# Kernel optimization log

Measured on AMD Instinct MI355X. Metric: run time of the kernel, lower is better.

Reference implementation:

```python
import jax, jax.numpy as jnp
import numpy as np
from jax import lax

B, C, N, T, K = 16, 64, 512, 64, 3
EPS = 1e-5


def _bn(x, g, b):
    # training-mode BatchNorm2d over (B, H=N, W=T) per channel
    m = jnp.mean(x, axis=(0, 2, 3), keepdims=True)
    v = jnp.var(x, axis=(0, 2, 3), keepdims=True)
    return (x - m) * lax.rsqrt(v + EPS) * g[None, :, None, None] + b[None, :, None, None]


def _conv(x, w, b, pad):
    y = lax.conv_general_dilated(x, w, (1, 1), ((0, 0), pad),
                                 dimension_numbers=('NCHW', 'OIHW', 'NCHW'))
    return y + b[None, :, None, None]


def setup_inputs() -> dict:
    key = jax.random.key(0)
    ks = jax.random.split(key, 8)
    xav = lambda k, sh, fi, fo: jax.random.normal(k, sh, jnp.float32) * np.sqrt(2.0 / (fi + fo))
    return {
        'x': jax.random.normal(ks[0], (B, C, N, T), jnp.float32),
        'adj_mx': jax.random.normal(ks[1], (K, N, N), jnp.float32) / np.sqrt(N),
        'cheb_w': xav(ks[2], (K, C, C), C, C),
        'cheb_b': jnp.zeros((C,), jnp.float32),
        'w1': xav(ks[3], (C, C, 1, 3), 3 * C, 3 * C),
        'b1': jnp.zeros((C,), jnp.float32),
        'g1': jnp.ones((C,), jnp.float32),
        'be1': jnp.zeros((C,), jnp.float32),
        'w2': xav(ks[4], (C, C, 1, 3), 3 * C, 3 * C),
        'b2': jnp.zeros((C,), jnp.float32),
        'g2': jnp.ones((C,), jnp.float32),
        'be2': jnp.zeros((C,), jnp.float32),
        'gate_w': xav(ks[5], (C, 2 * C, 1, 1), 2 * C, C),
        'gate_b': jnp.zeros((C,), jnp.float32),
        'res_w': xav(ks[6], (C, C, 1, 1), C, C),
        'res_b': jnp.zeros((C,), jnp.float32),
        'g3': jnp.ones((C,), jnp.float32),
        'be3': jnp.zeros((C,), jnp.float32),
    }


def _forward(x, adj_mx, cheb_w, cheb_b, w1, b1, g1, be1, w2, b2, g2, be2,
             gate_w, gate_b, res_w, res_b, g3, be3):
    # ChebFilterBlock: out[b,o,n,t] = sum_{k,i,m} x[b,i,m,t] adj[k,m,n] W[k,i,o] + bias
    spatial = jnp.einsum('bimt,kmn,kio->bont', x, adj_mx, cheb_w) \
              + cheb_b[None, :, None, None]
    # temporal branch: two (1,3) convs with BN+ReLU
    t = jax.nn.relu(_bn(_conv(x, w1, b1, (1, 1)), g1, be1))
    t = jax.nn.relu(_bn(_conv(t, w2, b2, (1, 1)), g2, be2))
    # gated fusion
    comb = jnp.concatenate([spatial, t], axis=1)
    gate = jax.nn.sigmoid(_conv(comb, gate_w, gate_b, (0, 0)))
    res = _conv(x, res_w, res_b, (0, 0))
    out = gate * spatial + (1.0 - gate) * t + res
    return _bn(out, g3, be3)


def reference(x, adj_mx, cheb_w, cheb_b, w1, b1, g1, be1, w2, b2, g2, be2,
              gate_w, gate_b, res_w, res_b, g3, be3):
    return _forward(x, adj_mx, cheb_w, cheb_b, w1, b1, g1, be1, w2, b2, g2, be2,
                    gate_w, gate_b, res_w, res_b, g3, be3)
```

## Files before the change

kernel.cpp:

```cpp
#include <hip/hip_runtime.h>
#include <hip/hip_bf16.h>
#include <cstdint>

#define BB 16
#define CC 64
#define NN 512
#define TT 64
#define KCH 3
#define PP (BB*NN*TT)
#define EPSB 1e-5f

typedef __bf16 bf16;
typedef __bf16 bf16x8 __attribute__((ext_vector_type(8)));
typedef __bf16 bf16x4 __attribute__((ext_vector_type(4)));
typedef float  f32x4  __attribute__((ext_vector_type(4)));

#define MFMA16(A,Bv,Cv) __builtin_amdgcn_mfma_f32_16x16x32_bf16((A),(Bv),(Cv),0,0,0)

__device__ __forceinline__ void gload_lds16(const bf16* g, bf16* l){
  __builtin_amdgcn_global_load_lds(
      (const __attribute__((address_space(1))) void*)g,
      (__attribute__((address_space(3))) void*)l, 16, 0, 0);
}

__global__ __launch_bounds__(256) void k_prep(const float* __restrict__ adj,
    const float* __restrict__ w1, const float* __restrict__ w2,
    const float* __restrict__ cw, const float* __restrict__ gw,
    const float* __restrict__ rw, bf16* __restrict__ adjb,
    bf16* __restrict__ w1p, bf16* __restrict__ w2p, bf16* __restrict__ cp,
    bf16* __restrict__ gp, bf16* __restrict__ rp){
  int blk = blockIdx.x, tid = threadIdx.x;
  if (blk < 3072){
    int idx = blk*256 + tid;
    int m = idx & 511, n = (idx >> 9) & 511, k = idx >> 18;
    adjb[idx] = (bf16)adj[((size_t)(k*512 + m))*512 + n];
    return;
  }
  int e0 = (blk - 3072)*256 + tid;
  if (e0 < 12288){
    int e = e0;
    int j = e&7, lane = (e>>3)&63, cf = (e>>9)&3, ks = e>>11;
    int k = ks*32 + (lane>>4)*8 + j, col = cf*16 + (lane&15);
    int kk = k >> 6, i = k & 63;
    w1p[e] = (bf16)w1[(col*64 + i)*3 + kk];
    w2p[e] = (bf16)w2[(col*64 + i)*3 + kk];
    cp[e]  = (bf16)cw[((size_t)kk*64 + i)*64 + col];
  } else if (e0 < 20480){
    int e = e0 - 12288;
    int j = e&7, lane = (e>>3)&63, cf = (e>>9)&3, ks = e>>11;
    int k = ks*32 + (lane>>4)*8 + j, col = cf*16 + (lane&15);
    gp[e] = (bf16)gw[col*128 + k];
  } else {
    int e = e0 - 20480;
    int j = e&7, lane = (e>>3)&63, cf = (e>>9)&3, ks = e>>11;
    int k = ks*32 + (lane>>4)*8 + j, col = cf*16 + (lane&15);
    rp[e] = (bf16)rw[col*64 + k];
  }
}

__global__ __launch_bounds__(256) void k_xprep(const float* __restrict__ x,
    bf16* __restrict__ xlb, bf16* __restrict__ xmt){
  __shared__ bf16 T[32768];
  int bid = blockIdx.x;
  int b = bid >> 6, i0 = ((bid >> 3) & 7)*8, n0 = (bid & 7)*64;
  int tid = threadIdx.x;
  #pragma unroll 4
  for (int it = 0; it < 32; ++it){
    int flat = it*256 + tid;
    int t4 = flat & 15, n = (flat >> 4) & 63, i = flat >> 10;
    float4 v = *reinterpret_cast<const float4*>(
        x + ((size_t)((b*64 + i0 + i)*512) + (n0 + n))*64 + t4*4);
    int s = t4 ^ ((n + 2*i) & 15);
    bf16x4 pk; pk[0]=(bf16)v.x; pk[1]=(bf16)v.y; pk[2]=(bf16)v.z; pk[3]=(bf16)v.w;
    *reinterpret_cast<bf16x4*>(&T[(i*64 + n)*64 + s*4]) = pk;
  }
  __syncthreads();
  #pragma unroll 4
  for (int it = 0; it < 16; ++it){
    int flat = it*256 + tid;
    int mc = flat & 7, i = (flat >> 3) & 7, t = flat >> 6;
    bf16x8 o;
    #pragma unroll
    for (int e = 0; e < 8; ++e){
      int m = mc*8 + e;
      int s = (t >> 2) ^ ((m + 2*i) & 15);
      o[e] = T[(i*64 + m)*64 + s*4 + (t & 3)];
    }
    *reinterpret_cast<bf16x8*>(
        &xmt[((size_t)((b*64 + t)*64) + i0 + i)*512 + n0 + mc*8]) = o;
  }
  #pragma unroll 4
  for (int it = 0; it < 16; ++it){
    int flat = it*256 + tid;
    int t = flat & 63, n = flat >> 6;
    bf16x8 o;
    #pragma unroll
    for (int e = 0; e < 8; ++e){
      int s = (t >> 2) ^ ((n + 2*e) & 15);
      o[e] = T[(e*64 + n)*64 + s*4 + (t & 3)];
    }
    *reinterpret_cast<bf16x8*>(
        &xlb[(((size_t)b*512 + n0 + n)*64 + t)*64 + i0]) = o;
  }
}

__global__ __launch_bounds__(256,4) void k_conv(const bf16* __restrict__ in,
    const bf16* __restrict__ wp, bf16* __restrict__ outp, float* __restrict__ part,
    const float* __restrict__ sc, const float* __restrict__ sh){
  int tid = threadIdx.x, w = tid >> 6, l = tid & 63, l15 = l & 15, lg = l >> 4;
  int blk = blockIdx.x;
  size_t rowbase = (size_t)blk * 64;
  const bf16* xr = in + rowbase * 64;
  int t = w*16 + l15;
  f32x4 acc[4] = {};
  #pragma unroll
  for (int ks = 0; ks < 6; ++ks){
    int dt = ks >> 1, kh = ks & 1;
    int ts = t + dt - 1;
    bf16x8 a = {};
    if (ts >= 0 && ts < 64){
      a = *reinterpret_cast<const bf16x8*>(xr + ts*64 + kh*32 + lg*8);
      if (sc){
        int i0 = kh*32 + lg*8;
        #pragma unroll
        for (int e = 0; e < 8; ++e){
          float f = (float)a[e]*sc[i0+e] + sh[i0+e];
          a[e] = (bf16)fmaxf(f, 0.f);
        }
      }
    }
    #pragma unroll
    for (int cf = 0; cf < 4; ++cf){
      bf16x8 bfr = *reinterpret_cast<const bf16x8*>(wp + ((ks*4 + cf)*64 + l)*8);
      acc[cf] = MFMA16(a, bfr, acc[cf]);
    }
  }
  __shared__ float ssum[4][4][16], ssq[4][4][16];
  #pragma unroll
  for (int cf = 0; cf < 4; ++cf){
    int o = cf*16 + l15;
    float s = 0.f, q = 0.f;
    #pragma unroll
    for (int r = 0; r < 4; ++r){
      float vv = acc[cf][r];
      int to = w*16 + lg*4 + r;
      outp[(rowbase + to)*64 + o] = (bf16)vv;
      s += vv; q += vv*vv;
    }
    s += __shfl_xor(s, 16); s += __shfl_xor(s, 32);
    q += __shfl_xor(q, 16); q += __shfl_xor(q, 32);
    if (lg == 0){ ssum[w][cf][l15] = s; ssq[w][cf][l15] = q; }
  }
  __syncthreads();
  if (tid < 64){
    int cf = tid >> 4, c = tid & 15;
    float s = ssum[0][cf][c]+ssum[1][cf][c]+ssum[2][cf][c]+ssum[3][cf][c];
    float q = ssq[0][cf][c]+ssq[1][cf][c]+ssq[2][cf][c]+ssq[3][cf][c];
    part[(size_t)blk*128 + tid*2]     = s;
    part[(size_t)blk*128 + tid*2 + 1] = q;
  }
}

__global__ __launch_bounds__(256) void k_stats(const float* __restrict__ part, int nb,
    const float* __restrict__ g, const float* __restrict__ be,
    float* __restrict__ sc, float* __restrict__ sh){
  int c = blockIdx.x, tid = threadIdx.x;
  float s = 0.f, q = 0.f;
  for (int i = tid; i < nb; i += 256){
    s += part[(size_t)i*128 + c*2];
    q += part[(size_t)i*128 + c*2 + 1];
  }
  __shared__ float rs[256], rq[256];
  rs[tid] = s; rq[tid] = q; __syncthreads();
  for (int st = 128; st > 0; st >>= 1){
    if (tid < st){ rs[tid] += rs[tid+st]; rq[tid] += rq[tid+st]; }
    __syncthreads();
  }
  if (tid == 0){
    float cnt = (float)PP;
    float mean = rs[0]/cnt, var = rq[0]/cnt - mean*mean;
    float r = rsqrtf(var + EPSB);
    sc[c] = g[c]*r;
    sh[c] = be[c] - mean*g[c]*r;
  }
}

__global__ __launch_bounds__(512,2) void k_gemm1(const bf16* __restrict__ xmt,
    const bf16* __restrict__ adjb, const bf16* __restrict__ cp,
    const float* __restrict__ cb, bf16* __restrict__ spm){
  __shared__ __align__(16) bf16 LDS[32768];

  int tid = threadIdx.x, w = tid >> 6, l = tid & 63, l15 = l & 15, lg = l >> 4;
  int wm = w >> 2, wn2 = w & 3;

  int orig = blockIdx.x;
  int wg = (orig & 7) * 256 + (orig >> 3);
  int jt = wg >> 2, nt = wg & 3;
  int J0 = jt*128, N0 = nt*128;

  const bf16* aglob = xmt + (size_t)J0*512;
  const bf16* bglob = adjb + (size_t)N0*512;

  int srow = tid >> 3, scn = (tid & 7) ^ ((tid >> 3) & 7);
  size_t soff = (size_t)srow*512 + scn*8;

  int colx[2];
  #pragma unroll
  for (int ph = 0; ph < 2; ++ph) colx[ph] = ((ph*4 + lg) ^ (l15 & 7))*8;
  int aoff[4], boff[2];
  #pragma unroll
  for (int jf = 0; jf < 4; ++jf) aoff[jf] = (wm*64 + jf*16 + l15)*64;
  #pragma unroll
  for (int nf = 0; nf < 2; ++nf) boff[nf] = (wn2*32 + nf*16 + l15)*64;

  f32x4 acc[4][2];
  f32x4 acc2[2][4] = {};

  for (int kk = 0; kk < 3; ++kk){
    const bf16* bko = bglob + (size_t)kk*262144;
    #pragma unroll
    for (int jf = 0; jf < 4; ++jf)
      #pragma unroll
      for (int nf = 0; nf < 2; ++nf)
        acc[jf][nf] = (f32x4){0.f,0.f,0.f,0.f};

    gload_lds16(aglob + soff,          LDS + tid*8);
    gload_lds16(aglob + soff + 32768,  LDS + 4096 + tid*8);
    gload_lds16(bko   + soff,          LDS + 16384 + tid*8);
    gload_lds16(bko   + soff + 32768,  LDS + 16384 + 4096 + tid*8);

    for (int kt = 0; kt < 8; ++kt){
      int buf = kt & 1, nbuf = buf ^ 1;
      bf16* Ab = LDS + buf*8192;
      bf16* Bb = LDS + 16384 + buf*8192;
      int mnext = (kt+1)*64;
      #pragma unroll
      for (int ph = 0; ph < 2; ++ph){
        if (kt < 7){
          if (ph == 0){
            gload_lds16(aglob + soff + mnext,         LDS + nbuf*8192 + tid*8);
            gload_lds16(aglob + soff + 32768 + mnext, LDS + nbuf*8192 + 4096 + tid*8);
          } else {
            gload_lds16(bko + soff + mnext,           LDS + 16384 + nbuf*8192 + tid*8);
            gload_lds16(bko + soff + 32768 + mnext,   LDS + 16384 + nbuf*8192 + 4096 + tid*8);
          }
        }
        if (ph == 0){
          if (kt < 7) asm volatile("s_waitcnt vmcnt(2)" ::: "memory");
          else        asm volatile("s_waitcnt vmcnt(0)" ::: "memory");
        }
        __builtin_amdgcn_sched_barrier(0);
        __builtin_amdgcn_s_barrier();
        __builtin_amdgcn_sched_barrier(0);

        bf16x8 a[4], bfr[2];
        #pragma unroll
        for (int jf = 0; jf < 4; ++jf)
          a[jf] = *reinterpret_cast<const bf16x8*>(&Ab[aoff[jf] + colx[ph]]);
        #pragma unroll
        for (int nf = 0; nf < 2; ++nf)
          bfr[nf] = *reinterpret_cast<const bf16x8*>(&Bb[boff[nf] + colx[ph]]);

        __builtin_amdgcn_s_setprio(1);
        #pragma unroll
        for (int jf = 0; jf < 4; ++jf)
          #pragma unroll
          for (int nf = 0; nf < 2; ++nf)
            acc[jf][nf] = MFMA16(a[jf], bfr[nf], acc[jf][nf]);
        __builtin_amdgcn_s_setprio(0);

        asm volatile("s_waitcnt lgkmcnt(0)" ::: "memory");
        __builtin_amdgcn_sched_barrier(0);
        __builtin_amdgcn_s_barrier();
      }
    }

    char* VTb = (char*)LDS;
    #pragma unroll
    for (int jf = 0; jf < 4; ++jf){
      int jb16 = wm*8 + jf*2 + (lg >> 1);
      int jlow = lg & 1;
      #pragma unroll
      for (int nf = 0; nf < 2; ++nf){
        int n = wn2*32 + nf*16 + l15;
        bf16x4 pk;
        #pragma unroll
        for (int r = 0; r < 4; ++r) pk[r] = (bf16)acc[jf][nf][r];
        *reinterpret_cast<bf16x4*>(
            VTb + n*256 + ((jb16 ^ (n & 15)) << 4) + (jlow << 3)) = pk;
      }
    }
    asm volatile("s_waitcnt lgkmcnt(0)" ::: "memory");
    __builtin_amdgcn_sched_barrier(0);
    __builtin_amdgcn_s_barrier();

    {
      int tloc = w >> 2, nbase = (w & 3)*32;
      #pragma unroll
      for (int ks2 = 0; ks2 < 2; ++ks2){
        bf16x8 bc[4];
        #pragma unroll
        for (int cf = 0; cf < 4; ++cf)
          bc[cf] = *reinterpret_cast<const bf16x8*>(
              cp + (((kk*2 + ks2)*4 + cf)*64 + l)*8);
        #pragma unroll
        for (int rf2 = 0; rf2 < 2; ++rf2){
          int nloc = nbase + rf2*16 + l15;
          int jb16 = tloc*8 + ks2*4 + lg;
          bf16x8 a2 = *reinterpret_cast<const bf16x8*>(
              VTb + nloc*256 + ((jb16 ^ (nloc & 15)) << 4));
          #pragma unroll
          for (int cf = 0; cf < 4; ++cf)
            acc2[rf2][cf] = MFMA16(a2, bc[cf], acc2[rf2][cf]);
        }
      }
    }
    asm volatile("s_waitcnt lgkmcnt(0)" ::: "memory");
    __builtin_amdgcn_sched_barrier(0);
    __builtin_amdgcn_s_barrier();
  }

  __syncthreads();
  bf16* SP = LDS;
  float cbv[4];
  #pragma unroll
  for (int cf = 0; cf < 4; ++cf) cbv[cf] = cb[cf*16 + l15];
  {
    int tloc = w >> 2, nbase = (w & 3)*32;
    #pragma unroll
    for (int rf2 = 0; rf2 < 2; ++rf2){
      int rowb = tloc*128 + nbase + rf2*16 + lg*4;
      #pragma unroll
      for (int cf = 0; cf < 4; ++cf){
        int o = cf*16 + l15;
        #pragma unroll
        for (int r = 0; r < 4; ++r)
          SP[(rowb + r)*64 + o] = (bf16)(acc2[rf2][cf][r] + cbv[cf]);
      }
    }
  }
  __syncthreads();
  int b = jt >> 5, t0 = (jt & 31)*2;
  #pragma unroll
  for (int q = 0; q < 4; ++q){
    int flat = q*512 + tid;
    int row = flat >> 3, oc = (flat & 7)*8;
    int tl = row >> 7, n = N0 + (row & 127);
    bf16x8 vv = *reinterpret_cast<const bf16x8*>(&SP[row*64 + oc]);
    *reinterpret_cast<bf16x8*>(
        &spm[(((size_t)b*512 + n)*64 + (t0 + tl))*64 + oc]) = vv;
  }
}

__global__ __launch_bounds__(256,4) void k_fusion(const bf16* __restrict__ spm,
    const bf16* __restrict__ t2, const bf16* __restrict__ xlb,
    const bf16* __restrict__ gp, const bf16* __restrict__ rp,
    const float* __restrict__ sc2, const float* __restrict__ sh2,
    const float* __restrict__ gateb, bf16* __restrict__ pre,
    float* __restrict__ part){
  int tid = threadIdx.x, w = tid >> 6, l = tid & 63, l15 = l & 15, lg = l >> 4;
  int blk = blockIdx.x;
  int b = blk >> 9, n = blk & 511;
  size_t rowbase = (size_t)blk * 64;
  int t = w*16 + l15;
  f32x4 ag[4] = {}, ar[4] = {};
  #pragma unroll
  for (int ks = 0; ks < 4; ++ks){
    bf16x8 a;
    if (ks < 2){
      a = *reinterpret_cast<const bf16x8*>(spm + (rowbase + t)*64 + ks*32 + lg*8);
    } else {
      int i0 = (ks-2)*32 + lg*8;
      bf16x8 raw = *reinterpret_cast<const bf16x8*>(t2 + (rowbase + t)*64 + i0);
      #pragma unroll
      for (int e = 0; e < 8; ++e){
        float f = (float)raw[e]*sc2[i0+e] + sh2[i0+e];
        a[e] = (bf16)fmaxf(f, 0.f);
      }
    }
    #pragma unroll
    for (int cf = 0; cf < 4; ++cf){
      bf16x8 bfr = *reinterpret_cast<const bf16x8*>(gp + ((ks*4 + cf)*64 + l)*8);
      ag[cf] = MFMA16(a, bfr, ag[cf]);
    }
  }
  #pragma unroll
  for (int ks = 0; ks < 2; ++ks){
    bf16x8 a = *reinterpret_cast<const bf16x8*>(xlb + (rowbase + t)*64 + ks*32 + lg*8);
    #pragma unroll
    for (int cf = 0; cf < 4; ++cf){
      bf16x8 bfr = *reinterpret_cast<const bf16x8*>(rp + ((ks*4 + cf)*64 + l)*8);
      ar[cf] = MFMA16(a, bfr, ar[cf]);
    }
  }
  __shared__ float ssum[4][4][16], ssq[4][4][16];
  int tb = w*16 + lg*4;
  #pragma unroll
  for (int cf = 0; cf < 4; ++cf){
    int o = cf*16 + l15;
    float gb = gateb[o], sco = sc2[o], sho = sh2[o];
    float s = 0.f, q = 0.f;
    bf16x4 ov;
    #pragma unroll
    for (int r = 0; r < 4; ++r){
      size_t row = rowbase + tb + r;
      float z = ag[cf][r] + gb;
      float g = 1.f/(1.f + __expf(-z));
      float spv = (float)spm[row*64 + o];
      float tv  = (float)t2[row*64 + o];
      tv = fmaxf(tv*sco + sho, 0.f);
      float val = g*spv + (1.f - g)*tv + ar[cf][r];
      ov[r] = (bf16)val;
      s += val; q += val*val;
    }
    *reinterpret_cast<bf16x4*>(pre + (((size_t)b*64 + o)*512 + n)*64 + tb) = ov;
    s += __shfl_xor(s, 16); s += __shfl_xor(s, 32);
    q += __shfl_xor(q, 16); q += __shfl_xor(q, 32);
    if (lg == 0){ ssum[w][cf][l15] = s; ssq[w][cf][l15] = q; }
  }
  __syncthreads();
  if (tid < 64){
    int cf = tid >> 4, c = tid & 15;
    float s = ssum[0][cf][c]+ssum[1][cf][c]+ssum[2][cf][c]+ssum[3][cf][c];
    float q = ssq[0][cf][c]+ssq[1][cf][c]+ssq[2][cf][c]+ssq[3][cf][c];
    part[(size_t)blk*128 + tid*2]     = s;
    part[(size_t)blk*128 + tid*2 + 1] = q;
  }
}

__global__ __launch_bounds__(256) void k_bn3(const bf16* __restrict__ pre,
    float* __restrict__ out,
    const float* __restrict__ sc, const float* __restrict__ sh){
  size_t total8 = (size_t)BB*CC*NN*TT/8;
  for (size_t i8 = (size_t)blockIdx.x*256 + threadIdx.x; i8 < total8;
       i8 += (size_t)gridDim.x*256){
    bf16x8 v = reinterpret_cast<const bf16x8*>(pre)[i8];
    int o = (int)(i8 >> 12) & 63;
    float a = sc[o], bsh = sh[o];
    float4 r0, r1;
    r0.x = (float)v[0]*a + bsh; r0.y = (float)v[1]*a + bsh;
    r0.z = (float)v[2]*a + bsh; r0.w = (float)v[3]*a + bsh;
    r1.x = (float)v[4]*a + bsh; r1.y = (float)v[5]*a + bsh;
    r1.z = (float)v[6]*a + bsh; r1.w = (float)v[7]*a + bsh;
    reinterpret_cast<float4*>(out)[i8*2]     = r0;
    reinterpret_cast<float4*>(out)[i8*2 + 1] = r1;
  }
}

extern "C" void kernel_launch(void* const* d_in, const int* in_sizes, int n_in,
                              void* d_out, int out_size, void* d_ws, size_t ws_size,
                              hipStream_t stream){
  (void)in_sizes; (void)n_in; (void)out_size; (void)ws_size;
  const float* x   = (const float*)d_in[0];
  const float* adj = (const float*)d_in[1];
  const float* cw  = (const float*)d_in[2];
  const float* cb  = (const float*)d_in[3];
  const float* w1  = (const float*)d_in[4];
  const float* g1  = (const float*)d_in[6];
  const float* be1 = (const float*)d_in[7];
  const float* w2  = (const float*)d_in[8];
  const float* g2  = (const float*)d_in[10];
  const float* be2 = (const float*)d_in[11];
  const float* gw  = (const float*)d_in[12];
  const float* gb  = (const float*)d_in[13];
  const float* rw  = (const float*)d_in[14];
  const float* g3  = (const float*)d_in[16];
  const float* be3 = (const float*)d_in[17];
  float* out = (float*)d_out;

  char* ws = (char*)d_ws;
  size_t off = 0;
  auto alloc = [&](size_t bytes)->char*{
    char* p = ws + off; off += (bytes + 255) & ~(size_t)255; return p;
  };
  bf16* xlb  = (bf16*)alloc((size_t)PP*64*2);
  bf16* xmt  = (bf16*)alloc((size_t)PP*64*2);
  bf16* t1   = (bf16*)alloc((size_t)PP*64*2);
  bf16* t2   = (bf16*)alloc((size_t)PP*64*2);
  bf16* spm  = t1;
  bf16* pre  = xmt;
  bf16* adjb = (bf16*)alloc((size_t)KCH*512*512*2);
  bf16* w1p  = (bf16*)alloc(6*2048*2);
  bf16* w2p  = (bf16*)alloc(6*2048*2);
  bf16* cp   = (bf16*)alloc(6*2048*2);
  bf16* gp   = (bf16*)alloc(4*2048*2);
  bf16* rp   = (bf16*)alloc(2*2048*2);
  float* part = (float*)alloc((size_t)8192*128*4);
  float* s1sc = (float*)alloc(256); float* s1sh = (float*)alloc(256);
  float* s2sc = (float*)alloc(256); float* s2sh = (float*)alloc(256);
  float* s3sc = (float*)alloc(256); float* s3sh = (float*)alloc(256);

  k_prep <<<dim3(3168), dim3(256), 0, stream>>>(adj, w1, w2, cw, gw, rw,
                                                adjb, w1p, w2p, cp, gp, rp);
  k_xprep<<<dim3(1024), dim3(256), 0, stream>>>(x, xlb, xmt);

  k_conv <<<dim3(8192), dim3(256), 0, stream>>>(xlb, w1p, t1, part, nullptr, nullptr);
  k_stats<<<dim3(64),   dim3(256), 0, stream>>>(part, 8192, g1, be1, s1sc, s1sh);
  k_conv <<<dim3(8192), dim3(256), 0, stream>>>(t1, w2p, t2, part, s1sc, s1sh);
  k_stats<<<dim3(64),   dim3(256), 0, stream>>>(part, 8192, g2, be2, s2sc, s2sh);

  k_gemm1<<<dim3(2048), dim3(512), 0, stream>>>(xmt, adjb, cp, cb, spm);

  k_fusion<<<dim3(8192), dim3(256), 0, stream>>>(spm, t2, xlb, gp, rp,
                                                 s2sc, s2sh, gb, pre, part);
  k_stats<<<dim3(64),   dim3(256), 0, stream>>>(part, 8192, g3, be3, s3sc, s3sh);
  k_bn3  <<<dim3(2048), dim3(256), 0, stream>>>(pre, out, s3sc, s3sh);
}
```

Measured before the change: 549.0 us.

## Split spatial GEMM into halves co-scheduled with each temporal conv launch

The separate conv and Chebyshev GEMM kernels are merged into one heterogeneous kernel. The first 1024 blocks run half of the GEMM tiles and the remaining blocks run the (1,3) conv, with two conv rows per 512-thread block. The kernel is launched twice, once per conv layer, so the compute-bound GEMM can overlap with the memory-bound conv passes and one launch is removed. The spatial output now gets its own buffer instead of aliasing t1, which costs extra workspace. Conv blocks now carry the GEMM's 64 KB static LDS and 512-thread launch bounds, which may reduce conv occupancy.

```diff
diff --git a/kernel.cpp b/kernel.cpp
--- a/kernel.cpp
+++ b/kernel.cpp
@@ -104,63 +104,6 @@
   }
 }
 
-__global__ __launch_bounds__(256,4) void k_conv(const bf16* __restrict__ in,
-    const bf16* __restrict__ wp, bf16* __restrict__ outp, float* __restrict__ part,
-    const float* __restrict__ sc, const float* __restrict__ sh){
-  int tid = threadIdx.x, w = tid >> 6, l = tid & 63, l15 = l & 15, lg = l >> 4;
-  int blk = blockIdx.x;
-  size_t rowbase = (size_t)blk * 64;
-  const bf16* xr = in + rowbase * 64;
-  int t = w*16 + l15;
-  f32x4 acc[4] = {};
-  #pragma unroll
-  for (int ks = 0; ks < 6; ++ks){
-    int dt = ks >> 1, kh = ks & 1;
-    int ts = t + dt - 1;
-    bf16x8 a = {};
-    if (ts >= 0 && ts < 64){
-      a = *reinterpret_cast<const bf16x8*>(xr + ts*64 + kh*32 + lg*8);
-      if (sc){
-        int i0 = kh*32 + lg*8;
-        #pragma unroll
-        for (int e = 0; e < 8; ++e){
-          float f = (float)a[e]*sc[i0+e] + sh[i0+e];
-          a[e] = (bf16)fmaxf(f, 0.f);
-        }
-      }
-    }
-    #pragma unroll
-    for (int cf = 0; cf < 4; ++cf){
-      bf16x8 bfr = *reinterpret_cast<const bf16x8*>(wp + ((ks*4 + cf)*64 + l)*8);
-      acc[cf] = MFMA16(a, bfr, acc[cf]);
-    }
-  }
-  __shared__ float ssum[4][4][16], ssq[4][4][16];
-  #pragma unroll
-  for (int cf = 0; cf < 4; ++cf){
-    int o = cf*16 + l15;
-    float s = 0.f, q = 0.f;
-    #pragma unroll
-    for (int r = 0; r < 4; ++r){
-      float vv = acc[cf][r];
-      int to = w*16 + lg*4 + r;
-      outp[(rowbase + to)*64 + o] = (bf16)vv;
-      s += vv; q += vv*vv;
-    }
-    s += __shfl_xor(s, 16); s += __shfl_xor(s, 32);
-    q += __shfl_xor(q, 16); q += __shfl_xor(q, 32);
-    if (lg == 0){ ssum[w][cf][l15] = s; ssq[w][cf][l15] = q; }
-  }
-  __syncthreads();
-  if (tid < 64){
-    int cf = tid >> 4, c = tid & 15;
-    float s = ssum[0][cf][c]+ssum[1][cf][c]+ssum[2][cf][c]+ssum[3][cf][c];
-    float q = ssq[0][cf][c]+ssq[1][cf][c]+ssq[2][cf][c]+ssq[3][cf][c];
-    part[(size_t)blk*128 + tid*2]     = s;
-    part[(size_t)blk*128 + tid*2 + 1] = q;
-  }
-}
-
 __global__ __launch_bounds__(256) void k_stats(const float* __restrict__ part, int nb,
     const float* __restrict__ g, const float* __restrict__ be,
     float* __restrict__ sc, float* __restrict__ sh){
@@ -185,170 +128,241 @@
   }
 }
 
-__global__ __launch_bounds__(512,2) void k_gemm1(const bf16* __restrict__ xmt,
-    const bf16* __restrict__ adjb, const bf16* __restrict__ cp,
-    const float* __restrict__ cb, bf16* __restrict__ spm){
+__global__ __launch_bounds__(512,2) void k_fat(
+    const bf16* __restrict__ cin, const bf16* __restrict__ wp,
+    bf16* __restrict__ coutp, float* __restrict__ part,
+    const float* __restrict__ sc, const float* __restrict__ sh,
+    const bf16* __restrict__ xmt, const bf16* __restrict__ adjb,
+    const bf16* __restrict__ cp, const float* __restrict__ cb,
+    bf16* __restrict__ spm, int gofs){
   __shared__ __align__(16) bf16 LDS[32768];
 
-  int tid = threadIdx.x, w = tid >> 6, l = tid & 63, l15 = l & 15, lg = l >> 4;
-  int wm = w >> 2, wn2 = w & 3;
-
-  int orig = blockIdx.x;
-  int wg = (orig & 7) * 256 + (orig >> 3);
-  int jt = wg >> 2, nt = wg & 3;
-  int J0 = jt*128, N0 = nt*128;
-
-  const bf16* aglob = xmt + (size_t)J0*512;
-  const bf16* bglob = adjb + (size_t)N0*512;
-
-  int srow = tid >> 3, scn = (tid & 7) ^ ((tid >> 3) & 7);
-  size_t soff = (size_t)srow*512 + scn*8;
-
-  int colx[2];
-  #pragma unroll
-  for (int ph = 0; ph < 2; ++ph) colx[ph] = ((ph*4 + lg) ^ (l15 & 7))*8;
-  int aoff[4], boff[2];
-  #pragma unroll
-  for (int jf = 0; jf < 4; ++jf) aoff[jf] = (wm*64 + jf*16 + l15)*64;
-  #pragma unroll
-  for (int nf = 0; nf < 2; ++nf) boff[nf] = (wn2*32 + nf*16 + l15)*64;
-
-  f32x4 acc[4][2];
-  f32x4 acc2[2][4] = {};
-
-  for (int kk = 0; kk < 3; ++kk){
-    const bf16* bko = bglob + (size_t)kk*262144;
-    #pragma unroll
-    for (int jf = 0; jf < 4; ++jf)
-      #pragma unroll
-      for (int nf = 0; nf < 2; ++nf)
-        acc[jf][nf] = (f32x4){0.f,0.f,0.f,0.f};
-
-    gload_lds16(aglob + soff,          LDS + tid*8);
-    gload_lds16(aglob + soff + 32768,  LDS + 4096 + tid*8);
-    gload_lds16(bko   + soff,          LDS + 16384 + tid*8);
-    gload_lds16(bko   + soff + 32768,  LDS + 16384 + 4096 + tid*8);
-
-    for (int kt = 0; kt < 8; ++kt){
-      int buf = kt & 1, nbuf = buf ^ 1;
-      bf16* Ab = LDS + buf*8192;
-      bf16* Bb = LDS + 16384 + buf*8192;
-      int mnext = (kt+1)*64;
-      #pragma unroll
-      for (int ph = 0; ph < 2; ++ph){
-        if (kt < 7){
+  int blk = blockIdx.x;
+  int tid = threadIdx.x;
+
+  if (blk < 1024){
+    int w = tid >> 6, l = tid & 63, l15 = l & 15, lg = l >> 4;
+    int wm = w >> 2, wn2 = w & 3;
+
+    int gwg = blk + gofs;
+    int wg = (gwg & 7) * 256 + (gwg >> 3);
+    int jt = wg >> 2, nt = wg & 3;
+    int J0 = jt*128, N0 = nt*128;
+
+    const bf16* aglob = xmt + (size_t)J0*512;
+    const bf16* bglob = adjb + (size_t)N0*512;
+
+    int srow = tid >> 3, scn = (tid & 7) ^ ((tid >> 3) & 7);
+    size_t soff = (size_t)srow*512 + scn*8;
+
+    int colx[2];
+    #pragma unroll
+    for (int ph = 0; ph < 2; ++ph) colx[ph] = ((ph*4 + lg) ^ (l15 & 7))*8;
+    int aoff[4], boff[2];
+    #pragma unroll
+    for (int jf = 0; jf < 4; ++jf) aoff[jf] = (wm*64 + jf*16 + l15)*64;
+    #pragma unroll
+    for (int nf = 0; nf < 2; ++nf) boff[nf] = (wn2*32 + nf*16 + l15)*64;
+
+    f32x4 acc[4][2];
+    f32x4 acc2[2][4] = {};
+
+    for (int kk = 0; kk < 3; ++kk){
+      const bf16* bko = bglob + (size_t)kk*262144;
+      #pragma unroll
+      for (int jf = 0; jf < 4; ++jf)
+        #pragma unroll
+        for (int nf = 0; nf < 2; ++nf)
+          acc[jf][nf] = (f32x4){0.f,0.f,0.f,0.f};
+
+      gload_lds16(aglob + soff,          LDS + tid*8);
+      gload_lds16(aglob + soff + 32768,  LDS + 4096 + tid*8);
+      gload_lds16(bko   + soff,          LDS + 16384 + tid*8);
+      gload_lds16(bko   + soff + 32768,  LDS + 16384 + 4096 + tid*8);
+
+      for (int kt = 0; kt < 8; ++kt){
+        int buf = kt & 1, nbuf = buf ^ 1;
+        bf16* Ab = LDS + buf*8192;
+        bf16* Bb = LDS + 16384 + buf*8192;
+        int mnext = (kt+1)*64;
+        #pragma unroll
+        for (int ph = 0; ph < 2; ++ph){
+          if (kt < 7){
+            if (ph == 0){
+              gload_lds16(cin ? aglob + soff + mnext : aglob, LDS + nbuf*8192 + tid*8);
+              gload_lds16(aglob + soff + 32768 + mnext, LDS + nbuf*8192 + 4096 + tid*8);
+            } else {
+              gload_lds16(bko + soff + mnext,           LDS + 16384 + nbuf*8192 + tid*8);
+              gload_lds16(bko + soff + 32768 + mnext,   LDS + 16384 + nbuf*8192 + 4096 + tid*8);
+            }
+          }
           if (ph == 0){
-            gload_lds16(aglob + soff + mnext,         LDS + nbuf*8192 + tid*8);
-            gload_lds16(aglob + soff + 32768 + mnext, LDS + nbuf*8192 + 4096 + tid*8);
-          } else {
-            gload_lds16(bko + soff + mnext,           LDS + 16384 + nbuf*8192 + tid*8);
-            gload_lds16(bko + soff + 32768 + mnext,   LDS + 16384 + nbuf*8192 + 4096 + tid*8);
+            if (kt < 7) asm volatile("s_waitcnt vmcnt(2)" ::: "memory");
+            else        asm volatile("s_waitcnt vmcnt(0)" ::: "memory");
+          }
+          __builtin_amdgcn_sched_barrier(0);
+          __builtin_amdgcn_s_barrier();
+          __builtin_amdgcn_sched_barrier(0);
+
+          bf16x8 a[4], bfr[2];
+          #pragma unroll
+          for (int jf = 0; jf < 4; ++jf)
+            a[jf] = *reinterpret_cast<const bf16x8*>(&Ab[aoff[jf] + colx[ph]]);
+          #pragma unroll
+          for (int nf = 0; nf < 2; ++nf)
+            bfr[nf] = *reinterpret_cast<const bf16x8*>(&Bb[boff[nf] + colx[ph]]);
+
+          __builtin_amdgcn_s_setprio(1);
+          #pragma unroll
+          for (int jf = 0; jf < 4; ++jf)
+            #pragma unroll
+            for (int nf = 0; nf < 2; ++nf)
+              acc[jf][nf] = MFMA16(a[jf], bfr[nf], acc[jf][nf]);
+          __builtin_amdgcn_s_setprio(0);
+
+          asm volatile("s_waitcnt lgkmcnt(0)" ::: "memory");
+          __builtin_amdgcn_sched_barrier(0);
+          __builtin_amdgcn_s_barrier();
+        }
+      }
+
+      char* VTb = (char*)LDS;
+      #pragma unroll
+      for (int jf = 0; jf < 4; ++jf){
+        int jb16 = wm*8 + jf*2 + (lg >> 1);
+        int jlow = lg & 1;
+        #pragma unroll
+        for (int nf = 0; nf < 2; ++nf){
+          int n = wn2*32 + nf*16 + l15;
+          bf16x4 pk;
+          #pragma unroll
+          for (int r = 0; r < 4; ++r) pk[r] = (bf16)acc[jf][nf][r];
+          *reinterpret_cast<bf16x4*>(
+              VTb + n*256 + ((jb16 ^ (n & 15)) << 4) + (jlow << 3)) = pk;
+        }
+      }
+      asm volatile("s_waitcnt lgkmcnt(0)" ::: "memory");
+      __builtin_amdgcn_sched_barrier(0);
+      __builtin_amdgcn_s_barrier();
+
+      {
+        int tloc = w >> 2, nbase = (w & 3)*32;
+        #pragma unroll
+        for (int ks2 = 0; ks2 < 2; ++ks2){
+          bf16x8 bc[4];
+          #pragma unroll
+          for (int cf = 0; cf < 4; ++cf)
+            bc[cf] = *reinterpret_cast<const bf16x8*>(
+                cp + (((kk*2 + ks2)*4 + cf)*64 + l)*8);
+          #pragma unroll
+          for (int rf2 = 0; rf2 < 2; ++rf2){
+            int nloc = nbase + rf2*16 + l15;
+            int jb16 = tloc*8 + ks2*4 + lg;
+            bf16x8 a2 = *reinterpret_cast<const bf16x8*>(
+                VTb + nloc*256 + ((jb16 ^ (nloc & 15)) << 4));
+            #pragma unroll
+            for (int cf = 0; cf < 4; ++cf)
+              acc2[rf2][cf] = MFMA16(a2, bc[cf], acc2[rf2][cf]);
           }
         }
-        if (ph == 0){
-          if (kt < 7) asm volatile("s_waitcnt vmcnt(2)" ::: "memory");
-          else        asm volatile("s_waitcnt vmcnt(0)" ::: "memory");
-        }
-        __builtin_amdgcn_sched_barrier(0);
-        __builtin_amdgcn_s_barrier();
-        __builtin_amdgcn_sched_barrier(0);
-
-        bf16x8 a[4], bfr[2];
-        #pragma unroll
-        for (int jf = 0; jf < 4; ++jf)
-          a[jf] = *reinterpret_cast<const bf16x8*>(&Ab[aoff[jf] + colx[ph]]);
-        #pragma unroll
-        for (int nf = 0; nf < 2; ++nf)
-          bfr[nf] = *reinterpret_cast<const bf16x8*>(&Bb[boff[nf] + colx[ph]]);
-
-        __builtin_amdgcn_s_setprio(1);
-        #pragma unroll
-        for (int jf = 0; jf < 4; ++jf)
-          #pragma unroll
-          for (int nf = 0; nf < 2; ++nf)
-            acc[jf][nf] = MFMA16(a[jf], bfr[nf], acc[jf][nf]);
-        __builtin_amdgcn_s_setprio(0);
-
-        asm volatile("s_waitcnt lgkmcnt(0)" ::: "memory");
-        __builtin_amdgcn_sched_barrier(0);
-        __builtin_amdgcn_s_barrier();
-      }
-    }
-
-    char* VTb = (char*)LDS;
-    #pragma unroll
-    for (int jf = 0; jf < 4; ++jf){
-      int jb16 = wm*8 + jf*2 + (lg >> 1);
-      int jlow = lg & 1;
-      #pragma unroll
-      for (int nf = 0; nf < 2; ++nf){
-        int n = wn2*32 + nf*16 + l15;
-        bf16x4 pk;
-        #pragma unroll
-        for (int r = 0; r < 4; ++r) pk[r] = (bf16)acc[jf][nf][r];
-        *reinterpret_cast<bf16x4*>(
-            VTb + n*256 + ((jb16 ^ (n & 15)) << 4) + (jlow << 3)) = pk;
-      }
-    }
-    asm volatile("s_waitcnt lgkmcnt(0)" ::: "memory");
-    __builtin_amdgcn_sched_barrier(0);
-    __builtin_amdgcn_s_barrier();
-
+      }
+      asm volatile("s_waitcnt lgkmcnt(0)" ::: "memory");
+      __builtin_amdgcn_sched_barrier(0);
+      __builtin_amdgcn_s_barrier();
+    }
+
+    __syncthreads();
+    bf16* SP = LDS;
+    float cbv[4];
+    #pragma unroll
+    for (int cf = 0; cf < 4; ++cf) cbv[cf] = cb[cf*16 + l15];
     {
       int tloc = w >> 2, nbase = (w & 3)*32;
       #pragma unroll
-      for (int ks2 = 0; ks2 < 2; ++ks2){
-        bf16x8 bc[4];
+      for (int rf2 = 0; rf2 < 2; ++rf2){
+        int rowb = tloc*128 + nbase + rf2*16 + lg*4;
         #pragma unroll
-        for (int cf = 0; cf < 4; ++cf)
-          bc[cf] = *reinterpret_cast<const bf16x8*>(
-              cp + (((kk*2 + ks2)*4 + cf)*64 + l)*8);
-        #pragma unroll
-        for (int rf2 = 0; rf2 < 2; ++rf2){
-          int nloc = nbase + rf2*16 + l15;
-          int jb16 = tloc*8 + ks2*4 + lg;
-          bf16x8 a2 = *reinterpret_cast<const bf16x8*>(
-              VTb + nloc*256 + ((jb16 ^ (nloc & 15)) << 4));
-          #pragma unroll
-          for (int cf = 0; cf < 4; ++cf)
-            acc2[rf2][cf] = MFMA16(a2, bc[cf], acc2[rf2][cf]);
+        for (int cf = 0; cf < 4; ++cf){
+          int o = cf*16 + l15;
+          #pragma unroll
+          for (int r = 0; r < 4; ++r)
+            SP[(rowb + r)*64 + o] = (bf16)(acc2[rf2][cf][r] + cbv[cf]);
         }
       }
     }
-    asm volatile("s_waitcnt lgkmcnt(0)" ::: "memory");
-    __builtin_amdgcn_sched_barrier(0);
-    __builtin_amdgcn_s_barrier();
-  }
-
-  __syncthreads();
-  bf16* SP = LDS;
-  float cbv[4];
-  #pragma unroll
-  for (int cf = 0; cf < 4; ++cf) cbv[cf] = cb[cf*16 + l15];
-  {
-    int tloc = w >> 2, nbase = (w & 3)*32;
-    #pragma unroll
-    for (int rf2 = 0; rf2 < 2; ++rf2){
-      int rowb = tloc*128 + nbase + rf2*16 + lg*4;
+    __syncthreads();
+    int b = jt >> 5, t0 = (jt & 31)*2;
+    #pragma unroll
+    for (int q = 0; q < 4; ++q){
+      int flat = q*512 + tid;
+      int row = flat >> 3, oc = (flat & 7)*8;
+      int tl = row >> 7, n = N0 + (row & 127);
+      bf16x8 vv = *reinterpret_cast<const bf16x8*>(&SP[row*64 + oc]);
+      *reinterpret_cast<bf16x8*>(
+          &spm[(((size_t)b*512 + n)*64 + (t0 + tl))*64 + oc]) = vv;
+    }
+  } else {
+    int sub = tid >> 8, t8 = tid & 255;
+    int w = t8 >> 6, l = t8 & 63, l15 = l & 15, lg = l >> 4;
+    size_t bn = (size_t)(blk - 1024)*2 + sub;
+    size_t rowbase = bn * 64;
+    const bf16* xr = cin + rowbase * 64;
+    int t = w*16 + l15;
+    f32x4 acc[4] = {};
+    #pragma unroll
+    for (int ks = 0; ks < 6; ++ks){
+      int dt = ks >> 1, kh = ks & 1;
+      int ts = t + dt - 1;
+      bf16x8 a = {};
+      if (ts >= 0 && ts < 64){
+        a = *reinterpret_cast<const bf16x8*>(xr + ts*64 + kh*32 + lg*8);
+        if (sc){
+          int i0 = kh*32 + lg*8;
+          #pragma unroll
+          for (int e = 0; e < 8; ++e){
+            float f = (float)a[e]*sc[i0+e] + sh[i0+e];
+            a[e] = (bf16)fmaxf(f, 0.f);
+          }
+        }
+      }
       #pragma unroll
       for (int cf = 0; cf < 4; ++cf){
-        int o = cf*16 + l15;
-        #pragma unroll
-        for (int r = 0; r < 4; ++r)
-          SP[(rowb + r)*64 + o] = (bf16)(acc2[rf2][cf][r] + cbv[cf]);
-      }
-    }
-  }
-  __syncthreads();
-  int b = jt >> 5, t0 = (jt & 31)*2;
-  #pragma unroll
-  for (int q = 0; q < 4; ++q){
-    int flat = q*512 + tid;
-    int row = flat >> 3, oc = (flat & 7)*8;
-    int tl = row >> 7, n = N0 + (row & 127);
-    bf16x8 vv = *reinterpret_cast<const bf16x8*>(&SP[row*64 + oc]);
-    *reinterpret_cast<bf16x8*>(
-        &spm[(((size_t)b*512 + n)*64 + (t0 + tl))*64 + oc]) = vv;
+        bf16x8 bfr = *reinterpret_cast<const bf16x8*>(wp + ((ks*4 + cf)*64 + l)*8);
+        acc[cf] = MFMA16(a, bfr, acc[cf]);
+      }
+    }
+    float* ssum = (float*)LDS;
+    float* ssq  = ssum + 512;
+    #pragma unroll
+    for (int cf = 0; cf < 4; ++cf){
+      int o = cf*16 + l15;
+      float s = 0.f, q = 0.f;
+      #pragma unroll
+      for (int r = 0; r < 4; ++r){
+        float vv = acc[cf][r];
+        int to = w*16 + lg*4 + r;
+        coutp[(rowbase + to)*64 + o] = (bf16)vv;
+        s += vv; q += vv*vv;
+      }
+      s += __shfl_xor(s, 16); s += __shfl_xor(s, 32);
+      q += __shfl_xor(q, 16); q += __shfl_xor(q, 32);
+      if (lg == 0){
+        ssum[((sub*4 + w)*4 + cf)*16 + l15] = s;
+        ssq [((sub*4 + w)*4 + cf)*16 + l15] = q;
+      }
+    }
+    __syncthreads();
+    if (t8 < 64){
+      int cf = t8 >> 4, c = t8 & 15;
+      float s = 0.f, q = 0.f;
+      #pragma unroll
+      for (int ww = 0; ww < 4; ++ww){
+        s += ssum[((sub*4 + ww)*4 + cf)*16 + c];
+        q += ssq [((sub*4 + ww)*4 + cf)*16 + c];
+      }
+      part[bn*128 + t8*2]     = s;
+      part[bn*128 + t8*2 + 1] = q;
+    }
   }
 }
 
@@ -477,7 +491,7 @@
   bf16* xmt  = (bf16*)alloc((size_t)PP*64*2);
   bf16* t1   = (bf16*)alloc((size_t)PP*64*2);
   bf16* t2   = (bf16*)alloc((size_t)PP*64*2);
-  bf16* spm  = t1;
+  bf16* spm  = (bf16*)alloc((size_t)PP*64*2);
   bf16* pre  = xmt;
   bf16* adjb = (bf16*)alloc((size_t)KCH*512*512*2);
   bf16* w1p  = (bf16*)alloc(6*2048*2);
@@ -494,12 +508,14 @@
                                                 adjb, w1p, w2p, cp, gp, rp);
   k_xprep<<<dim3(1024), dim3(256), 0, stream>>>(x, xlb, xmt);
 
-  k_conv <<<dim3(8192), dim3(256), 0, stream>>>(xlb, w1p, t1, part, nullptr, nullptr);
+  k_fat  <<<dim3(5120), dim3(512), 0, stream>>>(xlb, w1p, t1, part,
+                                                nullptr, nullptr,
+                                                xmt, adjb, cp, cb, spm, 0);
   k_stats<<<dim3(64),   dim3(256), 0, stream>>>(part, 8192, g1, be1, s1sc, s1sh);
-  k_conv <<<dim3(8192), dim3(256), 0, stream>>>(t1, w2p, t2, part, s1sc, s1sh);
+  k_fat  <<<dim3(5120), dim3(512), 0, stream>>>(t1, w2p, t2, part,
+                                                s1sc, s1sh,
+                                                xmt, adjb, cp, cb, spm, 1024);
   k_stats<<<dim3(64),   dim3(256), 0, stream>>>(part, 8192, g2, be2, s2sc, s2sh);
-
-  k_gemm1<<<dim3(2048), dim3(512), 0, stream>>>(xmt, adjb, cp, cb, spm);
 
   k_fusion<<<dim3(8192), dim3(256), 0, stream>>>(spm, t2, xlb, gp, rp,
                                                  s2sc, s2sh, gb, pre, part);
```

Measured after the change: 601.5 us. +9.6%, slower.
